# Kernel tuning notes

Measured on AMD Instinct MI355X. Metric: run time of the kernel, lower is better.

The kernel has to match this reference:

```python
import jax, jax.numpy as jnp
import numpy as np

N, D, H = 2048, 64, 64  # num_nodes, in_channels, hidden_channels


def setup_inputs() -> dict:
    key = jax.random.key(0)
    k0, k1, k2 = jax.random.split(key, 3)
    z = jax.random.normal(k0, (N, D), dtype=jnp.float32)
    # torch.nn.Linear params: W [out, in], y = x @ W.T + b
    W1 = jax.random.normal(k1, (H, 2 * D), dtype=jnp.float32) * (1.0 / np.sqrt(2 * D)).astype(np.float32)
    b1 = jnp.zeros((H,), dtype=jnp.float32)
    W2 = jax.random.normal(k2, (1, H), dtype=jnp.float32) * (1.0 / np.sqrt(H)).astype(np.float32)
    b2 = jnp.zeros((1,), dtype=jnp.float32)
    return {"z": z, "W1": W1, "b1": b1, "W2": W2, "b2": b2}


def reference(z, W1, b1, W2, b2):
    # decode(): adj[i, j] = Linear2(relu(Linear1(cat(z[i], z[j]))))  (dropout off: eval mode)
    # Efficient form: split W1 so cat(z_i, z_j) @ W1.T = z_i @ Wa.T + z_j @ Wb.T,
    # avoiding materializing the [N, N, 2D] concat tensor.
    n, d = z.shape
    Wa, Wb = W1[:, :d], W1[:, d:]           # each [H, D]
    hi = z @ Wa.T                            # [N, H] contribution from row node i
    hj = z @ Wb.T                            # [N, H] contribution from col node j
    h = jax.nn.relu(hi[:, None, :] + hj[None, :, :] + b1)  # [N, N, H]
    adj = jnp.einsum('ijh,h->ij', h, W2[0]) + b2[0]         # [N, N]
    # self_loop_mask=True: zero out the diagonal after sigmoid
    probs = jax.nn.sigmoid(adj) * (1.0 - jnp.eye(n, dtype=adj.dtype))
    return probs
```

## Files before the change

### kernel.cpp

```cpp
#include <hip/hip_runtime.h>
#include <math.h>

#define NN 2048
#define DD 64
#define HH 64
#define TI 128
#define TJ 64

__global__ __launch_bounds__(256) void prep_kernel(
    const float* __restrict__ z, const float* __restrict__ W1,
    const float* __restrict__ b1, float* __restrict__ u, float* __restrict__ v) {
  __shared__ float zs[8 * DD];
  const int t = threadIdx.x;
  const int i0 = blockIdx.x * 8;
  if (t < 128) {
    reinterpret_cast<float4*>(zs)[t] =
        reinterpret_cast<const float4*>(z + (size_t)i0 * DD)[t];
  }
  __syncthreads();

  const int hs = t & 127;
  const int rg = t >> 7;
  const int h = hs & 63;
  const int side = hs >> 6;
  const float* wrow = W1 + h * (2 * DD) + side * DD;

  float acc0 = 0.f, acc1 = 0.f, acc2 = 0.f, acc3 = 0.f;
#pragma unroll
  for (int d4 = 0; d4 < DD / 4; ++d4) {
    const float4 wv = reinterpret_cast<const float4*>(wrow)[d4];
    const float* z0 = zs + (rg * 4 + 0) * DD + d4 * 4;
    const float* z1 = z0 + DD;
    const float* z2 = z1 + DD;
    const float* z3 = z2 + DD;
    acc0 = fmaf(z0[3], wv.w, fmaf(z0[2], wv.z, fmaf(z0[1], wv.y, fmaf(z0[0], wv.x, acc0))));
    acc1 = fmaf(z1[3], wv.w, fmaf(z1[2], wv.z, fmaf(z1[1], wv.y, fmaf(z1[0], wv.x, acc1))));
    acc2 = fmaf(z2[3], wv.w, fmaf(z2[2], wv.z, fmaf(z2[1], wv.y, fmaf(z2[0], wv.x, acc2))));
    acc3 = fmaf(z3[3], wv.w, fmaf(z3[2], wv.z, fmaf(z3[1], wv.y, fmaf(z3[0], wv.x, acc3))));
  }
  const float bias = side ? 0.0f : b1[h];
  float* dst = side ? v : u;
  const int ib = i0 + rg * 4;
  dst[(size_t)(ib + 0) * HH + h] = acc0 + bias;
  dst[(size_t)(ib + 1) * HH + h] = acc1 + bias;
  dst[(size_t)(ib + 2) * HH + h] = acc2 + bias;
  dst[(size_t)(ib + 3) * HH + h] = acc3 + bias;
}

__global__ __launch_bounds__(256) void pair_kernel(
    const float* __restrict__ u, const float* __restrict__ v,
    const float* __restrict__ W2, const float* __restrict__ b2,
    float* __restrict__ out) {
  __shared__ float su[HH * TI];
  __shared__ float sv[HH * TJ];

  const int t = threadIdx.x;
  const int i0 = blockIdx.y * TI;
  const int j0 = blockIdx.x * TJ;

  const int c4 = t & 15;
  const int rq = (t >> 4) * 4;
#pragma unroll
  for (int k = 0; k < 2; ++k) {
    const int row = rq + k * 64;
    const float* src = u + (size_t)(i0 + row) * HH + c4 * 4;
    const float4 a0 = *reinterpret_cast<const float4*>(src);
    const float4 a1 = *reinterpret_cast<const float4*>(src + HH);
    const float4 a2 = *reinterpret_cast<const float4*>(src + 2 * HH);
    const float4 a3 = *reinterpret_cast<const float4*>(src + 3 * HH);
    *reinterpret_cast<float4*>(&su[(c4 * 4 + 0) * TI + row]) = make_float4(a0.x, a1.x, a2.x, a3.x);
    *reinterpret_cast<float4*>(&su[(c4 * 4 + 1) * TI + row]) = make_float4(a0.y, a1.y, a2.y, a3.y);
    *reinterpret_cast<float4*>(&su[(c4 * 4 + 2) * TI + row]) = make_float4(a0.z, a1.z, a2.z, a3.z);
    *reinterpret_cast<float4*>(&su[(c4 * 4 + 3) * TI + row]) = make_float4(a0.w, a1.w, a2.w, a3.w);
  }
  {
    const float* src = v + (size_t)(j0 + rq) * HH + c4 * 4;
    const float4 a0 = *reinterpret_cast<const float4*>(src);
    const float4 a1 = *reinterpret_cast<const float4*>(src + HH);
    const float4 a2 = *reinterpret_cast<const float4*>(src + 2 * HH);
    const float4 a3 = *reinterpret_cast<const float4*>(src + 3 * HH);
    *reinterpret_cast<float4*>(&sv[(c4 * 4 + 0) * TJ + rq]) = make_float4(a0.x, a1.x, a2.x, a3.x);
    *reinterpret_cast<float4*>(&sv[(c4 * 4 + 1) * TJ + rq]) = make_float4(a0.y, a1.y, a2.y, a3.y);
    *reinterpret_cast<float4*>(&sv[(c4 * 4 + 2) * TJ + rq]) = make_float4(a0.z, a1.z, a2.z, a3.z);
    *reinterpret_cast<float4*>(&sv[(c4 * 4 + 3) * TJ + rq]) = make_float4(a0.w, a1.w, a2.w, a3.w);
  }
  __syncthreads();

  const int tx = t & 15;
  const int ty = t >> 4;

  float acc[8][4] = {};
#pragma unroll 4
  for (int h = 0; h < HH; ++h) {
    const float wh = W2[h];
    const float4 uaL = *reinterpret_cast<const float4*>(&su[h * TI + ty * 8]);
    const float4 uaH = *reinterpret_cast<const float4*>(&su[h * TI + ty * 8 + 4]);
    const float4 vbv = *reinterpret_cast<const float4*>(&sv[h * TJ + tx * 4]);
    const float ua[8] = {uaL.x, uaL.y, uaL.z, uaL.w, uaH.x, uaH.y, uaH.z, uaH.w};
    const float vb[4] = {vbv.x, vbv.y, vbv.z, vbv.w};
#pragma unroll
    for (int a = 0; a < 8; ++a) {
#pragma unroll
      for (int b = 0; b < 4; ++b) {
        float s = ua[a] + vb[b];
        s = fmaxf(s, 0.0f);
        acc[a][b] = fmaf(s, wh, acc[a][b]);
      }
    }
  }

  const float bb = b2[0];
#pragma unroll
  for (int a = 0; a < 8; ++a) {
    const int i = i0 + ty * 8 + a;
    float4 r;
    {
      const float x0 = acc[a][0] + bb;
      const float x1 = acc[a][1] + bb;
      const float x2 = acc[a][2] + bb;
      const float x3 = acc[a][3] + bb;
      r.x = 1.0f / (1.0f + __expf(-x0));
      r.y = 1.0f / (1.0f + __expf(-x1));
      r.z = 1.0f / (1.0f + __expf(-x2));
      r.w = 1.0f / (1.0f + __expf(-x3));
    }
    const int jb = j0 + tx * 4;
    if (i - jb >= 0 && i - jb < 4) {
      if (i - jb == 0) r.x = 0.0f;
      else if (i - jb == 1) r.y = 0.0f;
      else if (i - jb == 2) r.z = 0.0f;
      else r.w = 0.0f;
    }
    *reinterpret_cast<float4*>(out + (size_t)i * NN + jb) = r;
  }
}

extern "C" void kernel_launch(void* const* d_in, const int* in_sizes, int n_in,
                              void* d_out, int out_size, void* d_ws, size_t ws_size,
                              hipStream_t stream) {
  const float* z  = (const float*)d_in[0];
  const float* W1 = (const float*)d_in[1];
  const float* b1 = (const float*)d_in[2];
  const float* W2 = (const float*)d_in[3];
  const float* b2 = (const float*)d_in[4];
  float* out = (float*)d_out;

  float* u = (float*)d_ws;
  float* v = u + (size_t)NN * HH;

  prep_kernel<<<NN / 8, 256, 0, stream>>>(z, W1, b1, u, v);
  pair_kernel<<<dim3(NN / TJ, NN / TI), 256, 0, stream>>>(u, v, W2, b2, out);
}
```

Baseline: 93.76 us.

## Use relu(x)=(x+|x|)/2 identity with precomputed linear terms and transposed v

Rewrites relu(u_i+v_j) as half of (u_i+v_j) plus half of its absolute value, so the linear part collapses to per-row and per-column scalars a_i and b_j computed in a new prep2 kernel, and the inner loop becomes add, abs-modifier, fma. The pair kernel now keeps one row of u in registers per thread and reads a transposed v (vt) directly from global memory with uniform broadcast loads instead of staging tiles in shared memory. This trims per-element ALU work (max replaced by a free abs modifier) but adds a third kernel launch, extra workspace, heavy register use (64-element p array plus accumulators), and uncoalesced row-strided output stores per thread.

```diff
diff --git a/kernel.cpp b/kernel.cpp
--- a/kernel.cpp
+++ b/kernel.cpp
@@ -4,8 +4,6 @@
 #define NN 2048
 #define DD 64
 #define HH 64
-#define TI 128
-#define TJ 64
 
 __global__ __launch_bounds__(256) void prep_kernel(
     const float* __restrict__ z, const float* __restrict__ W1,
@@ -47,91 +45,120 @@
   dst[(size_t)(ib + 3) * HH + h] = acc3 + bias;
 }
 
-__global__ __launch_bounds__(256) void pair_kernel(
+__global__ __launch_bounds__(256) void prep2_kernel(
     const float* __restrict__ u, const float* __restrict__ v,
-    const float* __restrict__ W2, const float* __restrict__ b2,
-    float* __restrict__ out) {
-  __shared__ float su[HH * TI];
-  __shared__ float sv[HH * TJ];
+    const float* __restrict__ W2,
+    float* __restrict__ vt, float* __restrict__ a, float* __restrict__ b) {
+  __shared__ float lu[64][65];
+  __shared__ float lv[64][65];
+  const int t = threadIdx.x;
+  const int i0 = blockIdx.x * 64;
 
-  const int t = threadIdx.x;
-  const int i0 = blockIdx.y * TI;
-  const int j0 = blockIdx.x * TJ;
-
-  const int c4 = t & 15;
-  const int rq = (t >> 4) * 4;
 #pragma unroll
-  for (int k = 0; k < 2; ++k) {
-    const int row = rq + k * 64;
-    const float* src = u + (size_t)(i0 + row) * HH + c4 * 4;
-    const float4 a0 = *reinterpret_cast<const float4*>(src);
-    const float4 a1 = *reinterpret_cast<const float4*>(src + HH);
-    const float4 a2 = *reinterpret_cast<const float4*>(src + 2 * HH);
-    const float4 a3 = *reinterpret_cast<const float4*>(src + 3 * HH);
-    *reinterpret_cast<float4*>(&su[(c4 * 4 + 0) * TI + row]) = make_float4(a0.x, a1.x, a2.x, a3.x);
-    *reinterpret_cast<float4*>(&su[(c4 * 4 + 1) * TI + row]) = make_float4(a0.y, a1.y, a2.y, a3.y);
-    *reinterpret_cast<float4*>(&su[(c4 * 4 + 2) * TI + row]) = make_float4(a0.z, a1.z, a2.z, a3.z);
-    *reinterpret_cast<float4*>(&su[(c4 * 4 + 3) * TI + row]) = make_float4(a0.w, a1.w, a2.w, a3.w);
-  }
-  {
-    const float* src = v + (size_t)(j0 + rq) * HH + c4 * 4;
-    const float4 a0 = *reinterpret_cast<const float4*>(src);
-    const float4 a1 = *reinterpret_cast<const float4*>(src + HH);
-    const float4 a2 = *reinterpret_cast<const float4*>(src + 2 * HH);
-    const float4 a3 = *reinterpret_cast<const float4*>(src + 3 * HH);
-    *reinterpret_cast<float4*>(&sv[(c4 * 4 + 0) * TJ + rq]) = make_float4(a0.x, a1.x, a2.x, a3.x);
-    *reinterpret_cast<float4*>(&sv[(c4 * 4 + 1) * TJ + rq]) = make_float4(a0.y, a1.y, a2.y, a3.y);
-    *reinterpret_cast<float4*>(&sv[(c4 * 4 + 2) * TJ + rq]) = make_float4(a0.z, a1.z, a2.z, a3.z);
-    *reinterpret_cast<float4*>(&sv[(c4 * 4 + 3) * TJ + rq]) = make_float4(a0.w, a1.w, a2.w, a3.w);
+  for (int k = 0; k < 4; ++k) {
+    const int idx = t + k * 256;
+    const int row = idx >> 4;
+    const int c4 = idx & 15;
+    const float4 fu = *reinterpret_cast<const float4*>(u + (size_t)(i0 + row) * HH + c4 * 4);
+    const float4 fv = *reinterpret_cast<const float4*>(v + (size_t)(i0 + row) * HH + c4 * 4);
+    lu[row][c4 * 4 + 0] = fu.x; lu[row][c4 * 4 + 1] = fu.y;
+    lu[row][c4 * 4 + 2] = fu.z; lu[row][c4 * 4 + 3] = fu.w;
+    lv[row][c4 * 4 + 0] = fv.x; lv[row][c4 * 4 + 1] = fv.y;
+    lv[row][c4 * 4 + 2] = fv.z; lv[row][c4 * 4 + 3] = fv.w;
   }
   __syncthreads();
 
-  const int tx = t & 15;
-  const int ty = t >> 4;
+#pragma unroll
+  for (int k = 0; k < 4; ++k) {
+    const int idx = t + k * 256;
+    const int h = idx >> 4;
+    const int c4 = idx & 15;
+    const float4 o = make_float4(lv[c4 * 4 + 0][h], lv[c4 * 4 + 1][h],
+                                 lv[c4 * 4 + 2][h], lv[c4 * 4 + 3][h]);
+    *reinterpret_cast<float4*>(vt + (size_t)h * NN + i0 + c4 * 4) = o;
+  }
 
-  float acc[8][4] = {};
-#pragma unroll 4
-  for (int h = 0; h < HH; ++h) {
-    const float wh = W2[h];
-    const float4 uaL = *reinterpret_cast<const float4*>(&su[h * TI + ty * 8]);
-    const float4 uaH = *reinterpret_cast<const float4*>(&su[h * TI + ty * 8 + 4]);
-    const float4 vbv = *reinterpret_cast<const float4*>(&sv[h * TJ + tx * 4]);
-    const float ua[8] = {uaL.x, uaL.y, uaL.z, uaL.w, uaH.x, uaH.y, uaH.z, uaH.w};
-    const float vb[4] = {vbv.x, vbv.y, vbv.z, vbv.w};
+  {
+    const int r = t >> 2;
+    const int qd = t & 3;
+    float sa = 0.f, sb = 0.f;
 #pragma unroll
-    for (int a = 0; a < 8; ++a) {
+    for (int k = 0; k < 16; ++k) {
+      const int h = qd * 16 + k;
+      const float w = W2[h];
+      sa = fmaf(w, lu[r][h], sa);
+      sb = fmaf(w, lv[r][h], sb);
+    }
+    sa += __shfl_xor(sa, 1); sa += __shfl_xor(sa, 2);
+    sb += __shfl_xor(sb, 1); sb += __shfl_xor(sb, 2);
+    if (qd == 0) {
+      a[i0 + r] = 0.5f * sa;
+      b[i0 + r] = 0.5f * sb;
+    }
+  }
+}
+
+__global__ __launch_bounds__(128) void pair_kernel(
+    const float* __restrict__ u, const float* __restrict__ vt,
+    const float* __restrict__ a, const float* __restrict__ b,
+    const float* __restrict__ W2, const float* __restrict__ b2,
+    float* __restrict__ out) {
+  const int t = threadIdx.x;
+  const int i = blockIdx.y * 128 + t;
+  const int jbase = blockIdx.x * 64;
+
+  float p[64];
+  const float4* urow = reinterpret_cast<const float4*>(u + (size_t)i * HH);
 #pragma unroll
-      for (int b = 0; b < 4; ++b) {
-        float s = ua[a] + vb[b];
-        s = fmaxf(s, 0.0f);
-        acc[a][b] = fmaf(s, wh, acc[a][b]);
+  for (int k = 0; k < 16; ++k) {
+    const float4 f = urow[k];
+    p[4 * k + 0] = f.x; p[4 * k + 1] = f.y;
+    p[4 * k + 2] = f.z; p[4 * k + 3] = f.w;
+  }
+  const float ai = a[i];
+  const float bias2 = b2[0];
+
+  for (int s = 0; s < 4; ++s) {
+    const int j0 = jbase + s * 16;
+    float acc[16] = {};
+#pragma unroll
+    for (int h = 0; h < HH; ++h) {
+      const float wh = W2[h];
+      const float* vr = vt + (size_t)h * NN + j0;
+      const float4 q0 = *reinterpret_cast<const float4*>(vr);
+      const float4 q1 = *reinterpret_cast<const float4*>(vr + 4);
+      const float4 q2 = *reinterpret_cast<const float4*>(vr + 8);
+      const float4 q3 = *reinterpret_cast<const float4*>(vr + 12);
+      const float qq[16] = {q0.x, q0.y, q0.z, q0.w, q1.x, q1.y, q1.z, q1.w,
+                            q2.x, q2.y, q2.z, q2.w, q3.x, q3.y, q3.z, q3.w};
+#pragma unroll
+      for (int c = 0; c < 16; ++c) {
+        const float sm = p[h] + qq[c];
+        acc[c] = fmaf(wh, fabsf(sm), acc[c]);
       }
     }
-  }
 
-  const float bb = b2[0];
+    const float* br = b + j0;
+    const float4 bj0 = *reinterpret_cast<const float4*>(br);
+    const float4 bj1 = *reinterpret_cast<const float4*>(br + 4);
+    const float4 bj2 = *reinterpret_cast<const float4*>(br + 8);
+    const float4 bj3 = *reinterpret_cast<const float4*>(br + 12);
+    const float bj[16] = {bj0.x, bj0.y, bj0.z, bj0.w, bj1.x, bj1.y, bj1.z, bj1.w,
+                          bj2.x, bj2.y, bj2.z, bj2.w, bj3.x, bj3.y, bj3.z, bj3.w};
+
+    float r[16];
 #pragma unroll
-  for (int a = 0; a < 8; ++a) {
-    const int i = i0 + ty * 8 + a;
-    float4 r;
-    {
-      const float x0 = acc[a][0] + bb;
-      const float x1 = acc[a][1] + bb;
-      const float x2 = acc[a][2] + bb;
-      const float x3 = acc[a][3] + bb;
-      r.x = 1.0f / (1.0f + __expf(-x0));
-      r.y = 1.0f / (1.0f + __expf(-x1));
-      r.z = 1.0f / (1.0f + __expf(-x2));
-      r.w = 1.0f / (1.0f + __expf(-x3));
+    for (int c = 0; c < 16; ++c) {
+      const float x = ai + bj[c] + bias2 + 0.5f * acc[c];
+      const float sg = 1.0f / (1.0f + __expf(-x));
+      r[c] = (i == j0 + c) ? 0.0f : sg;
     }
-    const int jb = j0 + tx * 4;
-    if (i - jb >= 0 && i - jb < 4) {
-      if (i - jb == 0) r.x = 0.0f;
-      else if (i - jb == 1) r.y = 0.0f;
-      else if (i - jb == 2) r.z = 0.0f;
-      else r.w = 0.0f;
+    float* orow = out + (size_t)i * NN + j0;
+#pragma unroll
+    for (int c4 = 0; c4 < 4; ++c4) {
+      *reinterpret_cast<float4*>(orow + c4 * 4) =
+          make_float4(r[c4 * 4 + 0], r[c4 * 4 + 1], r[c4 * 4 + 2], r[c4 * 4 + 3]);
     }
-    *reinterpret_cast<float4*>(out + (size_t)i * NN + jb) = r;
   }
 }
 
@@ -145,9 +172,13 @@
   const float* b2 = (const float*)d_in[4];
   float* out = (float*)d_out;
 
-  float* u = (float*)d_ws;
-  float* v = u + (size_t)NN * HH;
+  float* u  = (float*)d_ws;
+  float* v  = u + (size_t)NN * HH;
+  float* vt = v + (size_t)NN * HH;
+  float* a  = vt + (size_t)NN * HH;
+  float* b  = a + NN;
 
   prep_kernel<<<NN / 8, 256, 0, stream>>>(z, W1, b1, u, v);
-  pair_kernel<<<dim3(NN / TJ, NN / TI), 256, 0, stream>>>(u, v, W2, b2, out);
+  prep2_kernel<<<NN / 64, 256, 0, stream>>>(u, v, W2, vt, a, b);
+  pair_kernel<<<dim3(NN / 64, NN / 128), 128, 0, stream>>>(u, vt, a, b, W2, b2, out);
 }
```

Result: slower. 145.9 us (+55.6%).

## Rewrite relu as half-sum plus abs with precomputed linear terms, enlarge tiles

Applied to the files above, without the earlier changes.

Uses relu(x)=0.5(x+|x|) so the linear parts of the W2-weighted sum are precomputed per node in the prep kernel via wavefront shuffle reductions. The pair kernel then only accumulates w*|u+v|, which lets abs fold into an instruction modifier and removes the max. The pair tile also grows to 128x128 with 512 threads and padded shared memory to improve reuse. The cost is extra workspace arrays and a small change in rounding behaviour.

```diff
diff --git a/kernel.cpp b/kernel.cpp
--- a/kernel.cpp
+++ b/kernel.cpp
@@ -4,12 +4,14 @@
 #define NN 2048
 #define DD 64
 #define HH 64
-#define TI 128
-#define TJ 64
+#define TILE 128
+#define TP (TILE + 4)
 
 __global__ __launch_bounds__(256) void prep_kernel(
     const float* __restrict__ z, const float* __restrict__ W1,
-    const float* __restrict__ b1, float* __restrict__ u, float* __restrict__ v) {
+    const float* __restrict__ b1, const float* __restrict__ W2,
+    float* __restrict__ u, float* __restrict__ v,
+    float* __restrict__ a, float* __restrict__ b) {
   __shared__ float zs[8 * DD];
   const int t = threadIdx.x;
   const int i0 = blockIdx.x * 8;
@@ -39,99 +41,108 @@
     acc3 = fmaf(z3[3], wv.w, fmaf(z3[2], wv.z, fmaf(z3[1], wv.y, fmaf(z3[0], wv.x, acc3))));
   }
   const float bias = side ? 0.0f : b1[h];
+  const float s0 = acc0 + bias, s1 = acc1 + bias, s2 = acc2 + bias, s3 = acc3 + bias;
   float* dst = side ? v : u;
   const int ib = i0 + rg * 4;
-  dst[(size_t)(ib + 0) * HH + h] = acc0 + bias;
-  dst[(size_t)(ib + 1) * HH + h] = acc1 + bias;
-  dst[(size_t)(ib + 2) * HH + h] = acc2 + bias;
-  dst[(size_t)(ib + 3) * HH + h] = acc3 + bias;
+  dst[(size_t)(ib + 0) * HH + h] = s0;
+  dst[(size_t)(ib + 1) * HH + h] = s1;
+  dst[(size_t)(ib + 2) * HH + h] = s2;
+  dst[(size_t)(ib + 3) * HH + h] = s3;
+
+  const float wh = W2[h];
+  float r0 = wh * s0, r1 = wh * s1, r2 = wh * s2, r3 = wh * s3;
+#pragma unroll
+  for (int m = 1; m < 64; m <<= 1) {
+    r0 += __shfl_xor(r0, m);
+    r1 += __shfl_xor(r1, m);
+    r2 += __shfl_xor(r2, m);
+    r3 += __shfl_xor(r3, m);
+  }
+  if ((t & 63) == 0) {
+    float* d2 = side ? b : a;
+    d2[ib + 0] = 0.5f * r0;
+    d2[ib + 1] = 0.5f * r1;
+    d2[ib + 2] = 0.5f * r2;
+    d2[ib + 3] = 0.5f * r3;
+  }
 }
 
-__global__ __launch_bounds__(256) void pair_kernel(
+__global__ __launch_bounds__(512, 2) void pair_kernel(
     const float* __restrict__ u, const float* __restrict__ v,
+    const float* __restrict__ a, const float* __restrict__ b,
     const float* __restrict__ W2, const float* __restrict__ b2,
     float* __restrict__ out) {
-  __shared__ float su[HH * TI];
-  __shared__ float sv[HH * TJ];
+  __shared__ float su[HH][TP];
+  __shared__ float sv[HH][TP];
 
   const int t = threadIdx.x;
-  const int i0 = blockIdx.y * TI;
-  const int j0 = blockIdx.x * TJ;
+  const int i0 = blockIdx.y * TILE;
+  const int j0 = blockIdx.x * TILE;
 
-  const int c4 = t & 15;
-  const int rq = (t >> 4) * 4;
-#pragma unroll
-  for (int k = 0; k < 2; ++k) {
-    const int row = rq + k * 64;
-    const float* src = u + (size_t)(i0 + row) * HH + c4 * 4;
-    const float4 a0 = *reinterpret_cast<const float4*>(src);
-    const float4 a1 = *reinterpret_cast<const float4*>(src + HH);
-    const float4 a2 = *reinterpret_cast<const float4*>(src + 2 * HH);
-    const float4 a3 = *reinterpret_cast<const float4*>(src + 3 * HH);
-    *reinterpret_cast<float4*>(&su[(c4 * 4 + 0) * TI + row]) = make_float4(a0.x, a1.x, a2.x, a3.x);
-    *reinterpret_cast<float4*>(&su[(c4 * 4 + 1) * TI + row]) = make_float4(a0.y, a1.y, a2.y, a3.y);
-    *reinterpret_cast<float4*>(&su[(c4 * 4 + 2) * TI + row]) = make_float4(a0.z, a1.z, a2.z, a3.z);
-    *reinterpret_cast<float4*>(&su[(c4 * 4 + 3) * TI + row]) = make_float4(a0.w, a1.w, a2.w, a3.w);
-  }
   {
-    const float* src = v + (size_t)(j0 + rq) * HH + c4 * 4;
-    const float4 a0 = *reinterpret_cast<const float4*>(src);
-    const float4 a1 = *reinterpret_cast<const float4*>(src + HH);
-    const float4 a2 = *reinterpret_cast<const float4*>(src + 2 * HH);
-    const float4 a3 = *reinterpret_cast<const float4*>(src + 3 * HH);
-    *reinterpret_cast<float4*>(&sv[(c4 * 4 + 0) * TJ + rq]) = make_float4(a0.x, a1.x, a2.x, a3.x);
-    *reinterpret_cast<float4*>(&sv[(c4 * 4 + 1) * TJ + rq]) = make_float4(a0.y, a1.y, a2.y, a3.y);
-    *reinterpret_cast<float4*>(&sv[(c4 * 4 + 2) * TJ + rq]) = make_float4(a0.z, a1.z, a2.z, a3.z);
-    *reinterpret_cast<float4*>(&sv[(c4 * 4 + 3) * TJ + rq]) = make_float4(a0.w, a1.w, a2.w, a3.w);
+    const int r = t >> 4;
+    const int c = t & 15;
+    const float* us = u + (size_t)(i0 + 4 * r) * HH + 4 * c;
+    const float4 a0 = *reinterpret_cast<const float4*>(us);
+    const float4 a1 = *reinterpret_cast<const float4*>(us + HH);
+    const float4 a2 = *reinterpret_cast<const float4*>(us + 2 * HH);
+    const float4 a3 = *reinterpret_cast<const float4*>(us + 3 * HH);
+    *reinterpret_cast<float4*>(&su[4 * c + 0][4 * r]) = make_float4(a0.x, a1.x, a2.x, a3.x);
+    *reinterpret_cast<float4*>(&su[4 * c + 1][4 * r]) = make_float4(a0.y, a1.y, a2.y, a3.y);
+    *reinterpret_cast<float4*>(&su[4 * c + 2][4 * r]) = make_float4(a0.z, a1.z, a2.z, a3.z);
+    *reinterpret_cast<float4*>(&su[4 * c + 3][4 * r]) = make_float4(a0.w, a1.w, a2.w, a3.w);
+    const float* vs = v + (size_t)(j0 + 4 * r) * HH + 4 * c;
+    const float4 c0 = *reinterpret_cast<const float4*>(vs);
+    const float4 c1 = *reinterpret_cast<const float4*>(vs + HH);
+    const float4 c2 = *reinterpret_cast<const float4*>(vs + 2 * HH);
+    const float4 c3 = *reinterpret_cast<const float4*>(vs + 3 * HH);
+    *reinterpret_cast<float4*>(&sv[4 * c + 0][4 * r]) = make_float4(c0.x, c1.x, c2.x, c3.x);
+    *reinterpret_cast<float4*>(&sv[4 * c + 1][4 * r]) = make_float4(c0.y, c1.y, c2.y, c3.y);
+    *reinterpret_cast<float4*>(&sv[4 * c + 2][4 * r]) = make_float4(c0.z, c1.z, c2.z, c3.z);
+    *reinterpret_cast<float4*>(&sv[4 * c + 3][4 * r]) = make_float4(c0.w, c1.w, c2.w, c3.w);
   }
   __syncthreads();
 
   const int tx = t & 15;
   const int ty = t >> 4;
 
-  float acc[8][4] = {};
+  float acc[4][8] = {};
 #pragma unroll 4
   for (int h = 0; h < HH; ++h) {
     const float wh = W2[h];
-    const float4 uaL = *reinterpret_cast<const float4*>(&su[h * TI + ty * 8]);
-    const float4 uaH = *reinterpret_cast<const float4*>(&su[h * TI + ty * 8 + 4]);
-    const float4 vbv = *reinterpret_cast<const float4*>(&sv[h * TJ + tx * 4]);
-    const float ua[8] = {uaL.x, uaL.y, uaL.z, uaL.w, uaH.x, uaH.y, uaH.z, uaH.w};
-    const float vb[4] = {vbv.x, vbv.y, vbv.z, vbv.w};
+    const float4 ua = *reinterpret_cast<const float4*>(&su[h][ty * 4]);
+    const float4 vb0 = *reinterpret_cast<const float4*>(&sv[h][tx * 8]);
+    const float4 vb1 = *reinterpret_cast<const float4*>(&sv[h][tx * 8 + 4]);
+    const float uav[4] = {ua.x, ua.y, ua.z, ua.w};
+    const float vbv[8] = {vb0.x, vb0.y, vb0.z, vb0.w, vb1.x, vb1.y, vb1.z, vb1.w};
 #pragma unroll
-    for (int a = 0; a < 8; ++a) {
+    for (int k = 0; k < 4; ++k) {
 #pragma unroll
-      for (int b = 0; b < 4; ++b) {
-        float s = ua[a] + vb[b];
-        s = fmaxf(s, 0.0f);
-        acc[a][b] = fmaf(s, wh, acc[a][b]);
+      for (int cc = 0; cc < 8; ++cc) {
+        acc[k][cc] = fmaf(wh, fabsf(uav[k] + vbv[cc]), acc[k][cc]);
       }
     }
   }
 
-  const float bb = b2[0];
+  const float bias2 = b2[0];
+  const float4 bj0 = *reinterpret_cast<const float4*>(b + j0 + tx * 8);
+  const float4 bj1 = *reinterpret_cast<const float4*>(b + j0 + tx * 8 + 4);
+  const float bj[8] = {bj0.x, bj0.y, bj0.z, bj0.w, bj1.x, bj1.y, bj1.z, bj1.w};
+
 #pragma unroll
-  for (int a = 0; a < 8; ++a) {
-    const int i = i0 + ty * 8 + a;
-    float4 r;
-    {
-      const float x0 = acc[a][0] + bb;
-      const float x1 = acc[a][1] + bb;
-      const float x2 = acc[a][2] + bb;
-      const float x3 = acc[a][3] + bb;
-      r.x = 1.0f / (1.0f + __expf(-x0));
-      r.y = 1.0f / (1.0f + __expf(-x1));
-      r.z = 1.0f / (1.0f + __expf(-x2));
-      r.w = 1.0f / (1.0f + __expf(-x3));
+  for (int k = 0; k < 4; ++k) {
+    const int i = i0 + ty * 4 + k;
+    const float ai = a[i];
+    float r[8];
+#pragma unroll
+    for (int cc = 0; cc < 8; ++cc) {
+      const float x = ai + bj[cc] + bias2 + 0.5f * acc[k][cc];
+      const float sg = 1.0f / (1.0f + __expf(-x));
+      r[cc] = (i == j0 + tx * 8 + cc) ? 0.0f : sg;
     }
-    const int jb = j0 + tx * 4;
-    if (i - jb >= 0 && i - jb < 4) {
-      if (i - jb == 0) r.x = 0.0f;
-      else if (i - jb == 1) r.y = 0.0f;
-      else if (i - jb == 2) r.z = 0.0f;
-      else r.w = 0.0f;
-    }
-    *reinterpret_cast<float4*>(out + (size_t)i * NN + jb) = r;
+    float* orow = out + (size_t)i * NN + j0 + tx * 8;
+    *reinterpret_cast<float4*>(orow) = make_float4(r[0], r[1], r[2], r[3]);
+    *reinterpret_cast<float4*>(orow + 4) = make_float4(r[4], r[5], r[6], r[7]);
   }
 }
 
@@ -147,7 +158,9 @@
 
   float* u = (float*)d_ws;
   float* v = u + (size_t)NN * HH;
+  float* a = v + (size_t)NN * HH;
+  float* b = a + NN;
 
-  prep_kernel<<<NN / 8, 256, 0, stream>>>(z, W1, b1, u, v);
-  pair_kernel<<<dim3(NN / TJ, NN / TI), 256, 0, stream>>>(u, v, W2, b2, out);
+  prep_kernel<<<NN / 8, 256, 0, stream>>>(z, W1, b1, W2, u, v, a, b);
+  pair_kernel<<<dim3(NN / TILE, NN / TILE), 512, 0, stream>>>(u, v, a, b, W2, b2, out);
 }
```

Result: no change. 92.39 us (-1.5%).
